# Optimization experiments

Hardware: AMD Instinct MI355X
Metric: run time of the kernel (lower is better)

Reference implementation:

```python
import jax, jax.numpy as jnp
import numpy as np

N = 50000       # nodes
E = 800000      # edges (avg degree 16)
IN_DIM = 256
OUT_DIM = 64
NEG_SLOPE = 0.01  # F.leaky_relu default


def setup_inputs() -> dict:
    key = jax.random.key(0)
    k1, k2, k3, k4, k5 = jax.random.split(key, 5)
    features = jax.random.normal(k1, (N, IN_DIM), dtype=jnp.float32)
    # xavier-normal-ish scaling for weights
    W = jax.random.normal(k2, (IN_DIM, OUT_DIM), dtype=jnp.float32) / np.sqrt(IN_DIM)
    a = jax.random.normal(k3, (2 * OUT_DIM,), dtype=jnp.float32) / np.sqrt(2 * OUT_DIM)
    src = jax.random.randint(k4, (E,), 0, N)
    dst = jax.random.randint(k5, (E,), 0, N)
    return {"features": features, "W": W, "a": a, "src": src, "dst": dst}


def reference(features, W, a, src, dst):
    # z = fc(dropout(features)); dropout p=0 / eval -> identity
    z = features @ W                               # [N, D]
    # attn_fc([z_src || z_dst]) == z_src @ a_l + z_dst @ a_r
    el = z @ a[:OUT_DIM]                           # [N]
    er = z @ a[OUT_DIM:]                           # [N]
    e = jax.nn.leaky_relu(el[src] + er[dst], NEG_SLOPE)  # [E]
    # segment softmax over incoming edges of each destination node
    m = jax.ops.segment_max(e, dst, num_segments=N)      # [N]
    ex = jnp.exp(e - m[dst])                              # [E]
    denom = jax.ops.segment_sum(ex, dst, num_segments=N)  # [N]
    safe_denom = jnp.where(denom == 0, 1.0, denom)
    alpha = ex / safe_denom[dst]                           # [E]
    # weighted aggregation of source features
    h = jax.ops.segment_sum(alpha[:, None] * z[src], dst, num_segments=N)  # [N, D]
    return jax.nn.elu(h)
```

## Files before the change

kernel.cpp:

```cpp
#include <hip/hip_runtime.h>
#include <math.h>
#include <stdint.h>


constexpr int IN_D   = 256;
constexpr int OUT_D  = 64;
constexpr int NBLK   = 256;
constexpr int NBMAX  = 1024;
constexpr int CAPE   = 4096;
constexpr int FWAVES = 16;

typedef _Float16 f16x8 __attribute__((ext_vector_type(8)));
typedef float    f32x4 __attribute__((ext_vector_type(4)));

__device__ __forceinline__ void gload_lds16(const void* g, void* l) {
    __builtin_amdgcn_global_load_lds(
        (const __attribute__((address_space(1))) uint32_t*)g,
        (__attribute__((address_space(3))) uint32_t*)l, 16, 0, 0);
}


__global__ __launch_bounds__(256) void k_count(const int* __restrict__ dst,
                                               int* __restrict__ blkcnt,
                                               int* __restrict__ cursor,
                                               int E, int nb, int chunk) {
    __shared__ int cnt[NBMAX];
    const int b = blockIdx.x, tid = threadIdx.x;
    if (b == 0 && tid == 0) *cursor = 0;
    for (int i = tid; i < nb; i += 256) cnt[i] = 0;
    __syncthreads();
    const int lo = b * chunk;
    const int hi = (lo + chunk < E) ? lo + chunk : E;
    const int nv = (hi - lo) & ~3;
    for (int e = lo + tid * 4; e < lo + nv; e += 1024) {
        int4 d4 = *(const int4*)&dst[e];
        atomicAdd(&cnt[d4.x >> 6], 1);
        atomicAdd(&cnt[d4.y >> 6], 1);
        atomicAdd(&cnt[d4.z >> 6], 1);
        atomicAdd(&cnt[d4.w >> 6], 1);
    }
    for (int e = lo + nv + tid; e < hi; e += 256) atomicAdd(&cnt[dst[e] >> 6], 1);
    __syncthreads();
    for (int i = tid; i < nb; i += 256) blkcnt[(size_t)b * NBMAX + i] = cnt[i];
}

__global__ __launch_bounds__(256) void k_bsum(int* __restrict__ blkcnt,
                                              int* __restrict__ total,
                                              int* __restrict__ bbase,
                                              int* __restrict__ cursor, int nb) {
    const int j = blockIdx.x * 256 + threadIdx.x;
    const int lane = threadIdx.x & 63;
    int run = 0;
    if (j < nb) {
        #pragma unroll 8
        for (int b = 0; b < NBLK; ++b) {
            int v = blkcnt[(size_t)b * NBMAX + j];
            blkcnt[(size_t)b * NBMAX + j] = run;
            run += v;
        }
    }
    const int runp = (run + 3) & ~3;
    int incl = runp;
    #pragma unroll
    for (int ofs = 1; ofs < 64; ofs <<= 1) {
        int u = __shfl_up(incl, ofs, 64);
        if (lane >= ofs) incl += u;
    }
    int base = 0;
    if (lane == 63) base = atomicAdd(cursor, incl);
    base = __shfl(base, 63, 64);
    if (j < nb) { total[j] = run; bbase[j] = base + incl - runp; }
}

__global__ __launch_bounds__(256) void k_bin(const int* __restrict__ dst,
                                             const int* __restrict__ src,
                                             const int* __restrict__ blkcnt,
                                             const int* __restrict__ bbase,
                                             uint32_t* __restrict__ binned,
                                             int E, int nb, int chunk) {
    __shared__ int cur[NBMAX];
    const int b = blockIdx.x, tid = threadIdx.x;
    for (int i = tid; i < nb; i += 256)
        cur[i] = bbase[i] + blkcnt[(size_t)b * NBMAX + i];
    __syncthreads();
    const int lo = b * chunk;
    const int hi = (lo + chunk < E) ? lo + chunk : E;
    const int nv = (hi - lo) & ~3;
    for (int e = lo + tid * 4; e < lo + nv; e += 1024) {
        int4 d4 = *(const int4*)&dst[e];
        int4 s4 = *(const int4*)&src[e];
        int p;
        p = atomicAdd(&cur[d4.x >> 6], 1); binned[p] = ((uint32_t)d4.x << 16) | (uint32_t)s4.x;
        p = atomicAdd(&cur[d4.y >> 6], 1); binned[p] = ((uint32_t)d4.y << 16) | (uint32_t)s4.y;
        p = atomicAdd(&cur[d4.z >> 6], 1); binned[p] = ((uint32_t)d4.z << 16) | (uint32_t)s4.z;
        p = atomicAdd(&cur[d4.w >> 6], 1); binned[p] = ((uint32_t)d4.w << 16) | (uint32_t)s4.w;
    }
    for (int e = lo + nv + tid; e < hi; e += 256) {
        const uint32_t d = (uint32_t)dst[e];
        const int pos = atomicAdd(&cur[d >> 6], 1);
        binned[pos] = (d << 16) | (uint32_t)src[e];
    }
}


__global__ void k_wconv(const float* __restrict__ W, _Float16* __restrict__ Wf) {
    int t = blockIdx.x * 256 + threadIdx.x;
    int j    = t & 7;
    int lane = (t >> 3) & 63;
    int ct   = (t >> 9) & 3;
    int kc   = t >> 11;
    int k = kc * 32 + (lane >> 4) * 8 + j;
    int c = ct * 16 + (lane & 15);
    Wf[t] = (_Float16)W[k * OUT_D + c];
}

__global__ __launch_bounds__(256) void k_gemmf16(
        const float* __restrict__ feat, const _Float16* __restrict__ Wf,
        const float* __restrict__ a,
        _Float16* __restrict__ z, float* __restrict__ el, float* __restrict__ er,
        int n)
{
    __shared__ __align__(16) _Float16 WfL[IN_D * OUT_D];

    const int tid  = threadIdx.x;
    const int lane = tid & 63;
    const int wv   = tid >> 6;
    const int row0 = blockIdx.x * 64 + wv * 16;
    const int kg   = lane >> 4;

    int gr = row0 + (lane & 15); if (gr > n - 1) gr = n - 1;
    const float* frow = feat + (size_t)gr * IN_D;
    float4 r0[8], r1[8];
    #pragma unroll
    for (int kc = 0; kc < 8; ++kc) {
        const float4* fp = (const float4*)(frow + kc * 32 + kg * 8);
        r0[kc] = fp[0];
        r1[kc] = fp[1];
    }

    #pragma unroll
    for (int i = 0; i < 8; ++i) {
        const char* gsrc = (const char*)Wf + (size_t)(i * 256 + tid) * 16;
        char* ldst = (char*)WfL + (size_t)(i * 256 + wv * 64) * 16;
        gload_lds16(gsrc, ldst);
    }
    __syncthreads();

    f32x4 acc[4];
    #pragma unroll
    for (int ct = 0; ct < 4; ++ct) acc[ct] = (f32x4){0.f, 0.f, 0.f, 0.f};

    #pragma unroll
    for (int kc = 0; kc < 8; ++kc) {
        f16x8 af;
        af[0] = (_Float16)r0[kc].x; af[1] = (_Float16)r0[kc].y;
        af[2] = (_Float16)r0[kc].z; af[3] = (_Float16)r0[kc].w;
        af[4] = (_Float16)r1[kc].x; af[5] = (_Float16)r1[kc].y;
        af[6] = (_Float16)r1[kc].z; af[7] = (_Float16)r1[kc].w;
        #pragma unroll
        for (int ct = 0; ct < 4; ++ct) {
            f16x8 bf = *(const f16x8*)&WfL[((kc * 4 + ct) * 64 + lane) * 8];
            acc[ct] = __builtin_amdgcn_mfma_f32_16x16x32_f16(af, bf, acc[ct], 0, 0, 0);
        }
    }

    const int col = lane & 15;
    float av[4], bv[4];
    #pragma unroll
    for (int ct = 0; ct < 4; ++ct) {
        av[ct] = a[ct * 16 + col];
        bv[ct] = a[OUT_D + ct * 16 + col];
    }
    #pragma unroll
    for (int i = 0; i < 4; ++i) {
        const int r = row0 + (lane >> 4) * 4 + i;
        float vl = 0.f, vr = 0.f;
        #pragma unroll
        for (int ct = 0; ct < 4; ++ct) {
            float zv = acc[ct][i];
            if (r < n) z[(size_t)r * OUT_D + ct * 16 + col] = (_Float16)zv;
            vl = fmaf(zv, av[ct], vl);
            vr = fmaf(zv, bv[ct], vr);
        }
        #pragma unroll
        for (int msk = 8; msk >= 1; msk >>= 1) {
            vl += __shfl_xor(vl, msk, 64);
            vr += __shfl_xor(vr, msk, 64);
        }
        if (col == 0 && r < n) { el[r] = vl; er[r] = vr; }
    }
}

__global__ __launch_bounds__(1024) void k_fagg(
        const uint32_t* __restrict__ binned, const int* __restrict__ bbase,
        const int* __restrict__ total,
        const _Float16* __restrict__ z, const float* __restrict__ el,
        const float* __restrict__ er, float* __restrict__ out, int n)
{
    __shared__ __align__(16) uint32_t pr[CAPE];
    __shared__ uint16_t adjs[CAPE + 4];
    __shared__ int fcnt[64], foff[64], fcur[64];
    __shared__ float exs[FWAVES][64];

    const int j   = blockIdx.x, tid = threadIdx.x;
    const int lane = tid & 63;
    const int wv   = tid >> 6;
    const int ebase = bbase[j];
    int ecnt = total[j]; if (ecnt > CAPE) ecnt = CAPE;

    const int nv4 = (ecnt + 3) >> 2;
    for (int i = tid; i < nv4; i += 1024)
        *(uint4*)&pr[i * 4] = *(const uint4*)&binned[ebase + i * 4];
    if (tid < 64) { fcnt[tid] = 0; fcur[tid] = 0; }
    __syncthreads();
    for (int i = tid; i < ecnt; i += 1024)
        atomicAdd(&fcnt[(pr[i] >> 16) & 63], 1);
    __syncthreads();
    if (tid < 64) {
        const int v = fcnt[tid];
        int incl = v;
        #pragma unroll
        for (int ofs = 1; ofs < 64; ofs <<= 1) {
            int u = __shfl_up(incl, ofs, 64);
            if (tid >= ofs) incl += u;
        }
        foff[tid] = incl - v;
    }
    __syncthreads();
    for (int i = tid; i < ecnt; i += 1024) {
        const uint32_t u = pr[i];
        const int ld = (u >> 16) & 63;
        const int r = atomicAdd(&fcur[ld], 1);
        adjs[foff[ld] + r] = (uint16_t)(u & 0xFFFFu);
    }
    if (tid < 4) adjs[ecnt + tid] = 0;
    __syncthreads();

    const int sub = lane >> 4;
    const int qc  = lane & 15;

    #pragma unroll
    for (int t = 0; t < 64 / FWAVES; ++t) {
        const int ld = wv * (64 / FWAVES) + t;
        const int d = j * 64 + ld;
        if (d >= n) continue;
        const int deg = fcnt[ld];
        const int sb  = foff[ld];
        const float erd = er[d];

        float m = -INFINITY, den = 0.f;
        float4 acc = {0.f, 0.f, 0.f, 0.f};
        for (int b0 = 0; b0 < deg; b0 += 64) {
            const int i = b0 + lane;
            float lgv = -INFINITY;
            if (i < deg) {
                const int s = adjs[sb + i];
                const float x = el[s] + erd;
                lgv = x > 0.f ? x : 0.01f * x;
            }
            float cm = lgv;
            #pragma unroll
            for (int msk = 32; msk >= 1; msk >>= 1) cm = fmaxf(cm, __shfl_xor(cm, msk, 64));
            const float newm = fmaxf(m, cm);
            const float ex = (i < deg) ? __expf(lgv - newm) : 0.f;
            exs[wv][lane] = ex;
            float sum = ex;
            #pragma unroll
            for (int msk = 32; msk >= 1; msk >>= 1) sum += __shfl_xor(sum, msk, 64);
            const float scale = __expf(m - newm);
            den = den * scale + sum;
            acc.x *= scale; acc.y *= scale; acc.z *= scale; acc.w *= scale;
            m = newm;
            asm volatile("s_waitcnt lgkmcnt(0)" ::: "memory");

            const int cd  = (deg - b0 < 64) ? deg - b0 : 64;
            const int nit = (cd + 3) >> 2;
            for (int q = 0; q < nit; ++q) {
                const int idx = 4 * q + sub;
                const float wq = exs[wv][idx];
                const int   sq = adjs[sb + b0 + idx];
                const _Float16* zp = &z[(size_t)sq * OUT_D + qc * 4];
                uint2 v = *(const uint2*)zp;
                const _Float16* hf = (const _Float16*)&v;
                acc.x = fmaf(wq, (float)hf[0], acc.x);
                acc.y = fmaf(wq, (float)hf[1], acc.y);
                acc.z = fmaf(wq, (float)hf[2], acc.z);
                acc.w = fmaf(wq, (float)hf[3], acc.w);
            }
        }
        #pragma unroll
        for (int msk = 16; msk <= 32; msk <<= 1) {
            acc.x += __shfl_xor(acc.x, msk, 64);
            acc.y += __shfl_xor(acc.y, msk, 64);
            acc.z += __shfl_xor(acc.z, msk, 64);
            acc.w += __shfl_xor(acc.w, msk, 64);
        }
        if (sub == 0) {
            const float inv = (deg > 0) ? 1.f / den : 0.f;
            float4 h;
            h.x = acc.x * inv; h.y = acc.y * inv; h.z = acc.z * inv; h.w = acc.w * inv;
            h.x = h.x > 0.f ? h.x : expm1f(h.x);
            h.y = h.y > 0.f ? h.y : expm1f(h.y);
            h.z = h.z > 0.f ? h.z : expm1f(h.z);
            h.w = h.w > 0.f ? h.w : expm1f(h.w);
            *(float4*)&out[(size_t)d * OUT_D + qc * 4] = h;
        }
    }
}

extern "C" void kernel_launch(void* const* d_in, const int* in_sizes, int n_in,
                              void* d_out, int out_size, void* d_ws, size_t ws_size,
                              hipStream_t stream) {
    const float* feat = (const float*)d_in[0];
    const float* W    = (const float*)d_in[1];
    const float* a    = (const float*)d_in[2];
    const int*   src  = (const int*)d_in[3];
    const int*   dst  = (const int*)d_in[4];
    const int n = in_sizes[0] / IN_D;
    const int E = in_sizes[3];
    float* out = (float*)d_out;

    const int nb = (n + 63) >> 6;
    const int chunk = (((E + NBLK - 1) / NBLK) + 3) & ~3;

    char* ws = (char*)d_ws;
    _Float16* z_h = (_Float16*)ws;    ws += (size_t)n * OUT_D * 2;
    float* el = (float*)ws;           ws += (size_t)n * 4;
    float* er = (float*)ws;           ws += (size_t)n * 4;
    int*  total = (int*)ws;           ws += (size_t)NBMAX * 4;
    int*  bbase = (int*)ws;           ws += (size_t)NBMAX * 4;
    int*  cursor = (int*)ws;          ws += 16;
    int*  blkcnt = (int*)ws;          ws += (size_t)NBLK * NBMAX * 4;
    uint32_t* binned = (uint32_t*)ws; ws += ((size_t)E + 4 * NBMAX) * 4;
    _Float16* Wf = (_Float16*)ws;

    k_count<<<NBLK, 256, 0, stream>>>(dst, blkcnt, cursor, E, nb, chunk);
    k_bsum<<<(nb + 255) / 256, 256, 0, stream>>>(blkcnt, total, bbase, cursor, nb);
    k_bin<<<NBLK, 256, 0, stream>>>(dst, src, blkcnt, bbase, binned, E, nb, chunk);
    k_wconv<<<IN_D * OUT_D / 256, 256, 0, stream>>>(W, Wf);
    k_gemmf16<<<(n + 63) / 64, 256, 0, stream>>>(feat, Wf, a, z_h, el, er, n);
    k_fagg<<<nb, 1024, 0, stream>>>(binned, bbase, total, z_h, el, er, out, n);
}
```

Measured before the change: 166.4 us.

## Assign one destination node per 16-lane group in aggregation kernel

```diff
diff --git a/kernel.cpp b/kernel.cpp
--- a/kernel.cpp
+++ b/kernel.cpp
@@ -8,7 +8,6 @@
 constexpr int NBLK   = 256;
 constexpr int NBMAX  = 1024;
 constexpr int CAPE   = 4096;
-constexpr int FWAVES = 16;
 
 typedef _Float16 f16x8 __attribute__((ext_vector_type(8)));
 typedef float    f32x4 __attribute__((ext_vector_type(4)));
@@ -198,9 +197,8 @@
         const float* __restrict__ er, float* __restrict__ out, int n)
 {
     __shared__ __align__(16) uint32_t pr[CAPE];
-    __shared__ uint16_t adjs[CAPE + 4];
+    __shared__ uint16_t adjs[CAPE];
     __shared__ int fcnt[64], foff[64], fcur[64];
-    __shared__ float exs[FWAVES][64];
 
     const int j   = blockIdx.x, tid = threadIdx.x;
     const int lane = tid & 63;
@@ -233,78 +231,64 @@
         const int r = atomicAdd(&fcur[ld], 1);
         adjs[foff[ld] + r] = (uint16_t)(u & 0xFFFFu);
     }
-    if (tid < 4) adjs[ecnt + tid] = 0;
-    __syncthreads();
-
-    const int sub = lane >> 4;
-    const int qc  = lane & 15;
-
-    #pragma unroll
-    for (int t = 0; t < 64 / FWAVES; ++t) {
-        const int ld = wv * (64 / FWAVES) + t;
-        const int d = j * 64 + ld;
-        if (d >= n) continue;
-        const int deg = fcnt[ld];
-        const int sb  = foff[ld];
-        const float erd = er[d];
-
-        float m = -INFINITY, den = 0.f;
-        float4 acc = {0.f, 0.f, 0.f, 0.f};
-        for (int b0 = 0; b0 < deg; b0 += 64) {
-            const int i = b0 + lane;
-            float lgv = -INFINITY;
-            if (i < deg) {
-                const int s = adjs[sb + i];
-                const float x = el[s] + erd;
-                lgv = x > 0.f ? x : 0.01f * x;
-            }
-            float cm = lgv;
-            #pragma unroll
-            for (int msk = 32; msk >= 1; msk >>= 1) cm = fmaxf(cm, __shfl_xor(cm, msk, 64));
-            const float newm = fmaxf(m, cm);
-            const float ex = (i < deg) ? __expf(lgv - newm) : 0.f;
-            exs[wv][lane] = ex;
-            float sum = ex;
-            #pragma unroll
-            for (int msk = 32; msk >= 1; msk >>= 1) sum += __shfl_xor(sum, msk, 64);
-            const float scale = __expf(m - newm);
-            den = den * scale + sum;
-            acc.x *= scale; acc.y *= scale; acc.z *= scale; acc.w *= scale;
-            m = newm;
-            asm volatile("s_waitcnt lgkmcnt(0)" ::: "memory");
-
-            const int cd  = (deg - b0 < 64) ? deg - b0 : 64;
-            const int nit = (cd + 3) >> 2;
-            for (int q = 0; q < nit; ++q) {
-                const int idx = 4 * q + sub;
-                const float wq = exs[wv][idx];
-                const int   sq = adjs[sb + b0 + idx];
-                const _Float16* zp = &z[(size_t)sq * OUT_D + qc * 4];
-                uint2 v = *(const uint2*)zp;
-                const _Float16* hf = (const _Float16*)&v;
-                acc.x = fmaf(wq, (float)hf[0], acc.x);
-                acc.y = fmaf(wq, (float)hf[1], acc.y);
-                acc.z = fmaf(wq, (float)hf[2], acc.z);
-                acc.w = fmaf(wq, (float)hf[3], acc.w);
-            }
-        }
-        #pragma unroll
-        for (int msk = 16; msk <= 32; msk <<= 1) {
-            acc.x += __shfl_xor(acc.x, msk, 64);
-            acc.y += __shfl_xor(acc.y, msk, 64);
-            acc.z += __shfl_xor(acc.z, msk, 64);
-            acc.w += __shfl_xor(acc.w, msk, 64);
-        }
-        if (sub == 0) {
-            const float inv = (deg > 0) ? 1.f / den : 0.f;
-            float4 h;
-            h.x = acc.x * inv; h.y = acc.y * inv; h.z = acc.z * inv; h.w = acc.w * inv;
-            h.x = h.x > 0.f ? h.x : expm1f(h.x);
-            h.y = h.y > 0.f ? h.y : expm1f(h.y);
-            h.z = h.z > 0.f ? h.z : expm1f(h.z);
-            h.w = h.w > 0.f ? h.w : expm1f(h.w);
-            *(float4*)&out[(size_t)d * OUT_D + qc * 4] = h;
-        }
+    __syncthreads();
+
+    const int g     = lane >> 4;
+    const int qc    = lane & 15;
+    const int gbase = lane & 48;
+
+    const int ld  = wv * 4 + g;
+    const int d   = j * 64 + ld;
+    const bool ok = (d < n);
+    const int deg = ok ? fcnt[ld] : 0;
+    const int sb  = ok ? foff[ld] : 0;
+    const float erd = ok ? er[d] : 0.f;
+
+    float m = -INFINITY, den = 0.f;
+    float4 acc = {0.f, 0.f, 0.f, 0.f};
+    for (int c0 = 0; c0 < deg; c0 += 16) {
+        const int i = c0 + qc;
+        int s = 0;
+        float lgv = -INFINITY;
+        if (i < deg) {
+            s = adjs[sb + i];
+            const float x = el[s] + erd;
+            lgv = x > 0.f ? x : 0.01f * x;
+        }
+        float cm = lgv;
+        #pragma unroll
+        for (int msk = 8; msk >= 1; msk >>= 1) cm = fmaxf(cm, __shfl_xor(cm, msk, 16));
+        const float newm = fmaxf(m, cm);
+        const float ex = (i < deg) ? __expf(lgv - newm) : 0.f;
+        float sum = ex;
+        #pragma unroll
+        for (int msk = 8; msk >= 1; msk >>= 1) sum += __shfl_xor(sum, msk, 16);
+        const float scale = __expf(m - newm);
+        den = den * scale + sum;
+        acc.x *= scale; acc.y *= scale; acc.z *= scale; acc.w *= scale;
+        m = newm;
+
+        const int cd = (deg - c0 < 16) ? deg - c0 : 16;
+        for (int q = 0; q < cd; ++q) {
+            const float wq = __shfl(ex, gbase + q, 64);
+            const int   sq = __shfl(s,  gbase + q, 64);
+            uint2 v = *(const uint2*)&z[(size_t)sq * OUT_D + qc * 4];
+            const _Float16* hf = (const _Float16*)&v;
+            acc.x = fmaf(wq, (float)hf[0], acc.x);
+            acc.y = fmaf(wq, (float)hf[1], acc.y);
+            acc.z = fmaf(wq, (float)hf[2], acc.z);
+            acc.w = fmaf(wq, (float)hf[3], acc.w);
+        }
+    }
+    if (ok) {
+        const float inv = (deg > 0) ? 1.f / den : 0.f;
+        float4 h;
+        h.x = acc.x * inv; h.y = acc.y * inv; h.z = acc.z * inv; h.w = acc.w * inv;
+        h.x = h.x > 0.f ? h.x : expm1f(h.x);
+        h.y = h.y > 0.f ? h.y : expm1f(h.y);
+        h.z = h.z > 0.f ? h.z : expm1f(h.z);
+        h.w = h.w > 0.f ? h.w : expm1f(h.w);
+        *(float4*)&out[(size_t)d * OUT_D + qc * 4] = h;
     }
 }
 
```

Result: faster. 154.8 us (-7.0%).
